# Optimization experiments

Hardware: AMD Instinct MI355X
Metric: run time of the kernel (lower is better)

Reference implementation:

```python
import jax, jax.numpy as jnp
import numpy as np

B, S, HID, NH = 4, 2048, 1024, 16
DH = HID // NH  # 64
SCALE = 1.0 / float(np.sqrt(DH))


def _linear_params(key, scale=0.02):
    kw, kb = jax.random.split(key)
    W = jax.random.normal(kw, (HID, HID), dtype=jnp.float32) * scale
    b = jax.random.normal(kb, (HID,), dtype=jnp.float32) * scale
    return W, b


def setup_inputs() -> dict:
    key = jax.random.key(0)
    ks = jax.random.split(key, 9)
    x = jax.random.normal(ks[0], (B, S, HID), dtype=jnp.float32)
    reasoning_mask = jax.random.uniform(ks[1], (B, S, 1, 1), dtype=jnp.float32)
    Wq, bq = _linear_params(ks[2])
    Wk, bk = _linear_params(ks[3])
    Wv, bv = _linear_params(ks[4])
    Wqr, bqr = _linear_params(ks[5])
    Wkr, bkr = _linear_params(ks[6])
    Wo, bo = _linear_params(ks[7])
    return {"x": x, "reasoning_mask": reasoning_mask,
            "Wq": Wq, "bq": bq, "Wk": Wk, "bk": bk, "Wv": Wv, "bv": bv,
            "Wqr": Wqr, "bqr": bqr, "Wkr": Wkr, "bkr": bkr, "Wo": Wo, "bo": bo}


def reference(x, reasoning_mask, Wq, bq, Wk, bk, Wv, bv, Wqr, bqr, Wkr, bkr, Wo, bo):
    # Projections: x @ W + b, then view (B, S, NH, DH)
    def proj(W, b):
        return (jnp.einsum('bsh,hd->bsd', x, W) + b).reshape(B, S, NH, DH)

    q = proj(Wq, bq)
    k = proj(Wk, bk)
    v = proj(Wv, bv)
    q_r = proj(Wqr, bqr)
    k_r = proj(Wkr, bkr)

    # Reasoning-gated blend of standard and reasoning projections
    q = q * (1.0 - reasoning_mask) + q_r * reasoning_mask
    k = k * (1.0 - reasoning_mask) + k_r * reasoning_mask

    # Faithful to source: matmul over the LAST two dims of (B,S,NH,DH),
    # i.e. per-token attention ACROSS HEADS -> scores shape (B,S,NH,NH)
    scores = jnp.einsum('bshd,bsed->bshe', q, k) * SCALE
    attn = jax.nn.softmax(scores, axis=-1)  # dropout is identity at eval
    out = jnp.einsum('bshe,bsed->bshd', attn, v)  # (B,S,NH,DH)

    # Faithful transpose(1,2) + contiguous view to (B, S, HID)
    out = jnp.transpose(out, (0, 2, 1, 3)).reshape(B, -1, HID)
    return jnp.einsum('bsh,hd->bsd', out, Wo) + bo
```

## Files before the change

kernel.cpp:

```cpp
#include <hip/hip_runtime.h>
#include <hip/hip_bf16.h>


typedef __attribute__((ext_vector_type(8))) short short8;
typedef __attribute__((ext_vector_type(4))) short short4v;
typedef __attribute__((ext_vector_type(4))) float f32x4;

#define HID 1024
#define NTOK 8192
#define WT_ELEMS (1024 * 1024)

__device__ __forceinline__ short f2bs(float f) {
  __hip_bfloat16 h = __float2bfloat16(f);
  return *reinterpret_cast<short*>(&h);
}
__device__ __forceinline__ float bs2f(short s) {
  __hip_bfloat16 h;
  *reinterpret_cast<short*>(&h) = s;
  return __bfloat162float(h);
}
__device__ __forceinline__ void gload16(const void* g, void* l) {
  __builtin_amdgcn_global_load_lds(
      (const __attribute__((address_space(1))) void*)g,
      (__attribute__((address_space(3))) void*)l, 16, 0, 0);
}

#define BAR() asm volatile("s_barrier" ::: "memory")
#define VMWAIT(N) asm volatile("s_waitcnt vmcnt(" #N ")" ::: "memory")
#define LGKMW(N) do { asm volatile("s_waitcnt lgkmcnt(" #N ")" ::: "memory"); \
                      __builtin_amdgcn_sched_barrier(0); } while (0)
#define SCB __builtin_amdgcn_sched_barrier(0)
#define PRIO1 __builtin_amdgcn_s_setprio(1)
#define PRIO0 __builtin_amdgcn_s_setprio(0)
#define MFMA16x16 __builtin_amdgcn_mfma_f32_16x16x32_bf16

__global__ __launch_bounds__(256) void prep_kernel(
    const float* __restrict__ W0, const float* __restrict__ W1,
    const float* __restrict__ W2, const float* __restrict__ W3,
    const float* __restrict__ W4, const float* __restrict__ W5,
    const float* __restrict__ X, short* __restrict__ WT, short* __restrict__ XB)
{
  __shared__ short sT[64][68];
  const int bid = blockIdx.x, tid = threadIdx.x;
  if (bid < 1536) {
    const int z = bid >> 8, rem = bid & 255;
    const float* W = z == 0 ? W0 : z == 1 ? W1 : z == 2 ? W2 : z == 3 ? W3
                   : z == 4 ? W4 : W5;
    short* OUT = WT + (size_t)z * WT_ELEMS;
    const int k0 = (rem & 15) * 64, n0 = (rem >> 4) * 64;
    #pragma unroll
    for (int i = 0; i < 4; i++) {
      const int li = tid + i * 256;
      const int kr = li >> 4, c4 = (li & 15) << 2;
      const f32x4 wv = *reinterpret_cast<const f32x4*>(&W[(size_t)(k0 + kr) * HID + n0 + c4]);
      short4v s4;
      #pragma unroll
      for (int j = 0; j < 4; j++) s4[j] = f2bs(wv[j]);
      *reinterpret_cast<short4v*>(&sT[kr][c4]) = s4;
    }
    __syncthreads();
    #pragma unroll
    for (int i = 0; i < 4; i++) {
      const int li = tid + i * 256;
      const int nr = li >> 4, k4 = (li & 15) << 2;
      short4v o;
      #pragma unroll
      for (int j = 0; j < 4; j++) o[j] = sT[k4 + j][nr];
      const int kcol = (k0 + k4) ^ ((nr & 7) << 3);
      *reinterpret_cast<short4v*>(&OUT[(size_t)(n0 + nr) * HID + kcol]) = o;
    }
  } else {
    const int gid = (bid - 1536) * 256 + tid;
    const int row = gid >> 7, kc = (gid & 127) << 3;
    const f32x4 a = *reinterpret_cast<const f32x4*>(&X[(size_t)row * HID + kc]);
    const f32x4 b = *reinterpret_cast<const f32x4*>(&X[(size_t)row * HID + kc + 4]);
    short8 s;
    #pragma unroll
    for (int j = 0; j < 4; j++) { s[j] = f2bs(a[j]); s[4 + j] = f2bs(b[j]); }
    const int phys = (kc & ~63) | ((kc & 63) ^ ((row & 7) << 3));
    *reinterpret_cast<short8*>(&XB[(size_t)row * HID + phys]) = s;
  }
}

__global__ __launch_bounds__(512, 2) void gated8_kernel(
    const short* __restrict__ XB, const short* __restrict__ WTbase,
    const float* __restrict__ bq, const float* __restrict__ bqr,
    const float* __restrict__ bk, const float* __restrict__ bkr,
    const float* __restrict__ MASK,
    __hip_bfloat16* __restrict__ qg, __hip_bfloat16* __restrict__ kg)
{
  __shared__ short lA[2][256][64];
  __shared__ short lB1[2][128][64];
  __shared__ short lB2[2][128][64];

  const int d = blockIdx.x;
  const int bx = d & 31, byz = d >> 5;
  const int by = byz & 7, z = byz >> 3;

  const short* W1T = WTbase + (size_t)(2 * z) * WT_ELEMS;
  const short* W2T = W1T + WT_ELEMS;
  const float* B1b = z ? bk : bq;
  const float* B2b = z ? bkr : bqr;
  __hip_bfloat16* OUT = z ? kg : qg;

  const int m0 = bx * 256, n0 = by * 128;
  const int tid = threadIdx.x, lane = tid & 63, w = tid >> 6;
  const int wr = (w >> 1) * 64, wc = (w & 1) * 64;
  const int lrow = lane & 15, lkhi = (lane >> 4) << 3;
  const int swz = (lrow & 7) << 3;
  const int srow = lane >> 3, scol = (lane & 7) << 3;

  f32x4 acc1[4][4] = {}, acc2[4][4] = {};
  short8 bf1k[4], bf2k[4], bf1b[4];
  short8 afA0, afA1, afA2, afA3;
  short8 afB0, afB1, afB2, afB3;

  auto stA2 = [&](int slot, int kt, int i0) {
    const int k0 = kt * 64;
    #pragma unroll
    for (int i = 0; i < 2; i++) {
      const int chunk = w * 4 + i0 + i;
      gload16(&XB[(size_t)(m0 + chunk * 8 + srow) * HID + k0 + scol],
              &lA[slot][chunk * 8][0]);
    }
  };
  auto stB1s = [&](int slot, int kt) {
    const int k0 = kt * 64;
    #pragma unroll
    for (int i = 0; i < 2; i++) {
      const int chunk = w * 2 + i;
      gload16(&W1T[(size_t)(n0 + chunk * 8 + srow) * HID + k0 + scol],
              &lB1[slot][chunk * 8][0]);
    }
  };
  auto stB2s = [&](int slot, int kt) {
    const int k0 = kt * 64;
    #pragma unroll
    for (int i = 0; i < 2; i++) {
      const int chunk = w * 2 + i;
      gload16(&W2T[(size_t)(n0 + chunk * 8 + srow) * HID + k0 + scol],
              &lB2[slot][chunk * 8][0]);
    }
  };
  auto rdA = [&](int s, int m, int kk) -> short8 {
    const int lk = (kk * 32 + lkhi) ^ swz;
    return *reinterpret_cast<const short8*>(&lA[s][wr + m * 16 + lrow][lk]);
  };

#define RDB1(DST, S, KK)                                                              \
  _Pragma("unroll")                                                                   \
  for (int n = 0; n < 4; n++) {                                                       \
    const int lk = ((KK) * 32 + lkhi) ^ swz;                                          \
    DST[n] = *reinterpret_cast<const short8*>(&lB1[S][wc + n * 16 + lrow][lk]);       \
  }
#define RDB2(DST, S, KK)                                                              \
  _Pragma("unroll")                                                                   \
  for (int n = 0; n < 4; n++) {                                                       \
    const int lk = ((KK) * 32 + lkhi) ^ swz;                                          \
    DST[n] = *reinterpret_cast<const short8*>(&lB2[S][wc + n * 16 + lrow][lk]);       \
  }
#define MMC1(A0, A1, A2, A3, BF)                                          \
  _Pragma("unroll")                                                       \
  for (int n = 0; n < 4; n++) {                                           \
    acc1[0][n] = MFMA16x16(A0, BF[n], acc1[0][n], 0, 0, 0);               \
    acc1[1][n] = MFMA16x16(A1, BF[n], acc1[1][n], 0, 0, 0);               \
    acc1[2][n] = MFMA16x16(A2, BF[n], acc1[2][n], 0, 0, 0);               \
    acc1[3][n] = MFMA16x16(A3, BF[n], acc1[3][n], 0, 0, 0);               \
  }
#define MMC2(A0, A1, A2, A3, BF)                                          \
  _Pragma("unroll")                                                       \
  for (int n = 0; n < 4; n++) {                                           \
    acc2[0][n] = MFMA16x16(A0, BF[n], acc2[0][n], 0, 0, 0);               \
    acc2[1][n] = MFMA16x16(A1, BF[n], acc2[1][n], 0, 0, 0);               \
    acc2[2][n] = MFMA16x16(A2, BF[n], acc2[2][n], 0, 0, 0);               \
    acc2[3][n] = MFMA16x16(A3, BF[n], acc2[3][n], 0, 0, 0);               \
  }
#define GTILE(S, SN, TS)                                                 \
  afA0 = rdA(S, 0, 0); afA1 = rdA(S, 1, 0);                              \
  afA2 = rdA(S, 2, 0); afA3 = rdA(S, 3, 0);                              \
  SCB;                                                                   \
  RDB1(bf1k, S, 0);                                                      \
  SCB;                                                                   \
  RDB2(bf2k, S, 0);                                                      \
  SCB;                                                                   \
  afB0 = rdA(S, 0, 1); afB1 = rdA(S, 1, 1);                              \
  afB2 = rdA(S, 2, 1); afB3 = rdA(S, 3, 1);                              \
  SCB;                                                                   \
  RDB1(bf1b, S, 1);                                                      \
  SCB;                                                                   \
  stA2(SN, TS, 0); stA2(SN, TS, 2); stB1s(SN, TS); stB2s(SN, TS);        \
  SCB;                                                                   \
  LGKMW(12);                                                             \
  PRIO1; MMC1(afA0, afA1, afA2, afA3, bf1k) PRIO0; SCB;                  \
  LGKMW(8);                                                              \
  PRIO1; MMC2(afA0, afA1, afA2, afA3, bf2k) PRIO0; SCB;                  \
  RDB2(bf2k, S, 1);                                                      \
  SCB;                                                                   \
  LGKMW(4);                                                              \
  PRIO1; MMC1(afB0, afB1, afB2, afB3, bf1b) PRIO0; SCB;                  \
  LGKMW(0);                                                              \
  PRIO1; MMC2(afB0, afB1, afB2, afB3, bf2k) PRIO0; SCB;                  \
  VMWAIT(0);                                                             \
  BAR();

  stA2(0, 0, 0); stA2(0, 0, 2); stB1s(0, 0); stB2s(0, 0);
  VMWAIT(0);
  BAR();

  #pragma unroll 1
  for (int i = 0; i < 16; i++) {
    const int S = i & 1, SN = S ^ 1;
    const int TS = (i < 15) ? i + 1 : 15;
    GTILE(S, SN, TS)
  }
#undef GTILE
#undef MMC1
#undef MMC2
#undef RDB1
#undef RDB2

  #pragma unroll
  for (int m = 0; m < 4; m++) {
    const int rbase = m0 + wr + m * 16 + ((lane >> 4) << 2);
    #pragma unroll
    for (int n = 0; n < 4; n++) {
      const int col = n0 + wc + n * 16 + lrow;
      const float bias1 = B1b[col];
      const float bias2 = B2b[col];
      #pragma unroll
      for (int r = 0; r < 4; r++) {
        const int row = rbase + r;
        const float mk = MASK[row];
        const float val = (acc1[m][n][r] + bias1) * (1.f - mk) +
                          (acc2[m][n][r] + bias2) * mk;
        OUT[(size_t)row * HID + col] = __float2bfloat16(val);
      }
    }
  }
}

template<bool OUTF32>
__global__ __launch_bounds__(512, 2) void plain8_kernel(
    const short* __restrict__ A, const short* __restrict__ WT,
    const float* __restrict__ BIAS, void* __restrict__ OUTv)
{
  __shared__ short lA[3][256][64];
  __shared__ short lB[3][128][64];

  const int d = blockIdx.x;
  const int bx = d & 31, by = d >> 5;

  const int m0 = bx * 256, n0 = by * 128;
  const int tid = threadIdx.x, lane = tid & 63, w = tid >> 6;
  const int wr = (w >> 1) * 64, wc = (w & 1) * 64;
  const int lrow = lane & 15, lkhi = (lane >> 4) << 3;
  const int swz = (lrow & 7) << 3;
  const int srow = lane >> 3, scol = (lane & 7) << 3;

  f32x4 acc[4][4] = {};
  short8 paf[2][4], pbf[2][4];

  auto stTrip = [&](int slot, int kt, int t) {
    const int k0 = kt * 64;
    if (t == 0) {
      #pragma unroll
      for (int i = 0; i < 3; i++) {
        const int chunk = w * 4 + i;
        gload16(&A[(size_t)(m0 + chunk * 8 + srow) * HID + k0 + scol],
                &lA[slot][chunk * 8][0]);
      }
    } else {
      const int chunk = w * 4 + 3;
      gload16(&A[(size_t)(m0 + chunk * 8 + srow) * HID + k0 + scol],
              &lA[slot][chunk * 8][0]);
      #pragma unroll
      for (int i = 0; i < 2; i++) {
        const int bchunk = w * 2 + i;
        gload16(&WT[(size_t)(n0 + bchunk * 8 + srow) * HID + k0 + scol],
                &lB[slot][bchunk * 8][0]);
      }
    }
  };

#define RDP(S, KK)                                                                    \
  _Pragma("unroll")                                                                   \
  for (int m = 0; m < 4; m++) {                                                       \
    const int lk = ((KK) * 32 + lkhi) ^ swz;                                          \
    paf[KK][m] = *reinterpret_cast<const short8*>(&lA[S][wr + m * 16 + lrow][lk]);    \
    pbf[KK][m] = *reinterpret_cast<const short8*>(&lB[S][wc + m * 16 + lrow][lk]);    \
  }
#define PMM16(KK)                                                                     \
  _Pragma("unroll")                                                                   \
  for (int m = 0; m < 4; m++)                                                         \
    _Pragma("unroll")                                                                 \
    for (int n = 0; n < 4; n++)                                                       \
      acc[m][n] = MFMA16x16(paf[KK][m], pbf[KK][n], acc[KK == 0 ? m : m][n], 0, 0, 0);

  stTrip(0, 0, 0); stTrip(0, 0, 1);
  stTrip(1, 1, 0); stTrip(1, 1, 1);
  VMWAIT(6);
  BAR();

  int s = 0, s2 = 2;
  #pragma unroll 1
  for (int t = 0; t < 16; t++) {
    const int TS = (t < 14) ? t + 2 : 15;
    RDP(s, 0)
    SCB;
    RDP(s, 1)
    SCB;
    stTrip(s2, TS, 0); stTrip(s2, TS, 1);
    SCB;
    LGKMW(8);
    PRIO1; PMM16(0) PRIO0; SCB;
    LGKMW(0);
    PRIO1; PMM16(1) PRIO0; SCB;
    VMWAIT(6);
    BAR();
    s = (s == 2) ? 0 : s + 1;
    s2 = (s2 == 2) ? 0 : s2 + 1;
  }
#undef PMM16
#undef RDP

  #pragma unroll
  for (int m = 0; m < 4; m++) {
    const int rbase = m0 + wr + m * 16 + ((lane >> 4) << 2);
    #pragma unroll
    for (int n = 0; n < 4; n++) {
      const int col = n0 + wc + n * 16 + lrow;
      const float bias = BIAS[col];
      #pragma unroll
      for (int r = 0; r < 4; r++) {
        const float val = acc[m][n][r] + bias;
        const size_t oidx = (size_t)(rbase + r) * HID + col;
        if (OUTF32) ((float*)OUTv)[oidx] = val;
        else ((__hip_bfloat16*)OUTv)[oidx] = __float2bfloat16(val);
      }
    }
  }
}

__global__ __launch_bounds__(256) void attn_kernel(
    const __hip_bfloat16* __restrict__ Q, const __hip_bfloat16* __restrict__ K,
    const __hip_bfloat16* __restrict__ V, __hip_bfloat16* __restrict__ O)
{
  const int t = blockIdx.x;
  const int b = t >> 11, s = t & 2047;
  __shared__ float sQ[16][68], sK[16][68], sV[16][68];
  __shared__ float sA[16][17];
  const int tid = threadIdx.x;
  const size_t tb = (size_t)t * HID;

  {
    const int h = tid >> 4, d0 = (tid & 15) << 2;
    const int o = (h << 6) + d0;
    const short4v qv = *reinterpret_cast<const short4v*>(&((const short*)Q)[tb + o]);
    const short4v kv = *reinterpret_cast<const short4v*>(&((const short*)K)[tb + o]);
    const short4v vv = *reinterpret_cast<const short4v*>(&((const short*)V)[tb + o]);
    #pragma unroll
    for (int j = 0; j < 4; j++) {
      sQ[h][d0 + j] = bs2f(qv[j]);
      sK[h][d0 + j] = bs2f(kv[j]);
      sV[h][d0 + j] = bs2f(vv[j]);
    }
  }
  __syncthreads();

  const int h = tid >> 4, e = tid & 15;
  float sc = 0.f;
  #pragma unroll
  for (int dd = 0; dd < 64; dd++) sc += sQ[h][dd] * sK[e][dd];
  sc *= 0.125f;

  float mx = sc;
  mx = fmaxf(mx, __shfl_xor(mx, 1));
  mx = fmaxf(mx, __shfl_xor(mx, 2));
  mx = fmaxf(mx, __shfl_xor(mx, 4));
  mx = fmaxf(mx, __shfl_xor(mx, 8));
  const float p = __expf(sc - mx);
  float sm = p;
  sm += __shfl_xor(sm, 1);
  sm += __shfl_xor(sm, 2);
  sm += __shfl_xor(sm, 4);
  sm += __shfl_xor(sm, 8);
  sA[h][e] = p / sm;
  __syncthreads();

  const int row7 = (s >> 4) & 7;
  const size_t ob = ((size_t)b * 2048 + (s >> 4)) * HID + ((size_t)(s & 15) << 6);
  {
    const int hh = tid >> 4, d4 = (tid & 15) << 2;
    f32x4 o = {0.f, 0.f, 0.f, 0.f};
    #pragma unroll
    for (int e2 = 0; e2 < 16; e2++) {
      const float a = sA[hh][e2];
      #pragma unroll
      for (int j = 0; j < 4; j++) o[j] += a * sV[e2][d4 + j];
    }
    short4v ov;
    #pragma unroll
    for (int j = 0; j < 4; j++) ov[j] = f2bs(o[j]);
    *reinterpret_cast<short4v*>(
        &((short*)O)[ob + (size_t)hh * 128 * HID + (d4 ^ (row7 << 3))]) = ov;
  }
}

extern "C" void kernel_launch(void* const* d_in, const int* in_sizes, int n_in,
                              void* d_out, int out_size, void* d_ws, size_t ws_size,
                              hipStream_t stream) {
  (void)in_sizes; (void)n_in; (void)out_size; (void)ws_size;
  const float* x   = (const float*)d_in[0];
  const float* rm  = (const float*)d_in[1];
  const float* Wq  = (const float*)d_in[2];
  const float* bq  = (const float*)d_in[3];
  const float* Wk  = (const float*)d_in[4];
  const float* bk  = (const float*)d_in[5];
  const float* Wv  = (const float*)d_in[6];
  const float* bv  = (const float*)d_in[7];
  const float* Wqr = (const float*)d_in[8];
  const float* bqr = (const float*)d_in[9];
  const float* Wkr = (const float*)d_in[10];
  const float* bkr = (const float*)d_in[11];
  const float* Wo  = (const float*)d_in[12];
  const float* bo  = (const float*)d_in[13];

  char* ws = (char*)d_ws;
  short* wt = (short*)ws;
  __hip_bfloat16* qg = (__hip_bfloat16*)(ws + 12u * 1024 * 1024);
  __hip_bfloat16* vv = (__hip_bfloat16*)(ws + 28u * 1024 * 1024);
  __hip_bfloat16* ar = (__hip_bfloat16*)(ws + 44u * 1024 * 1024);
  short* xb = (short*)d_out;
  __hip_bfloat16* kg = (__hip_bfloat16*)((char*)d_out + 16u * 1024 * 1024);

  prep_kernel<<<dim3(5632), 256, 0, stream>>>(Wq, Wqr, Wk, Wkr, Wv, Wo, x, wt, xb);
  gated8_kernel<<<dim3(512), 512, 0, stream>>>(xb, wt, bq, bqr, bk, bkr, rm, qg, kg);
  plain8_kernel<false><<<dim3(256), 512, 0, stream>>>(xb, wt + (size_t)4 * WT_ELEMS, bv, vv);
  attn_kernel<<<dim3(NTOK), 256, 0, stream>>>(qg, kg, vv, ar);
  plain8_kernel<true><<<dim3(256), 512, 0, stream>>>((const short*)ar,
                                                     wt + (size_t)5 * WT_ELEMS, bo, d_out);
}
```

Measured before the change: 145.2 us.

## Merge V projection into gated Q/K projection launch and move barriers before last MFMA

```diff
diff --git a/kernel.cpp b/kernel.cpp
--- a/kernel.cpp
+++ b/kernel.cpp
@@ -82,26 +82,26 @@
   }
 }
 
-__global__ __launch_bounds__(512, 2) void gated8_kernel(
+__global__ __launch_bounds__(512, 2) void proj_kernel(
     const short* __restrict__ XB, const short* __restrict__ WTbase,
     const float* __restrict__ bq, const float* __restrict__ bqr,
     const float* __restrict__ bk, const float* __restrict__ bkr,
-    const float* __restrict__ MASK,
-    __hip_bfloat16* __restrict__ qg, __hip_bfloat16* __restrict__ kg)
+    const float* __restrict__ bv, const float* __restrict__ MASK,
+    __hip_bfloat16* __restrict__ qg, __hip_bfloat16* __restrict__ kg,
+    __hip_bfloat16* __restrict__ vg)
 {
   __shared__ short lA[2][256][64];
   __shared__ short lB1[2][128][64];
   __shared__ short lB2[2][128][64];
 
-  const int d = blockIdx.x;
-  const int bx = d & 31, byz = d >> 5;
-  const int by = byz & 7, z = byz >> 3;
-
-  const short* W1T = WTbase + (size_t)(2 * z) * WT_ELEMS;
+  const int z = blockIdx.z;
+  const int bx = blockIdx.x & 31, by = blockIdx.x >> 5;
+  const bool gated = (z < 2);
+  const short* W1T = WTbase + (size_t)(z == 2 ? 4 : 2 * z) * WT_ELEMS;
   const short* W2T = W1T + WT_ELEMS;
-  const float* B1b = z ? bk : bq;
-  const float* B2b = z ? bkr : bqr;
-  __hip_bfloat16* OUT = z ? kg : qg;
+  const float* B1b = z == 0 ? bq : z == 1 ? bk : bv;
+  const float* B2b = z == 0 ? bqr : bkr;
+  __hip_bfloat16* OUT = z == 0 ? qg : z == 1 ? kg : vg;
 
   const int m0 = bx * 256, n0 = by * 128;
   const int tid = threadIdx.x, lane = tid & 63, w = tid >> 6;
@@ -111,7 +111,7 @@
   const int srow = lane >> 3, scol = (lane & 7) << 3;
 
   f32x4 acc1[4][4] = {}, acc2[4][4] = {};
-  short8 bf1k[4], bf2k[4], bf1b[4];
+  short8 bfa[4], bfb[4];
   short8 afA0, afA1, afA2, afA3;
   short8 afB0, afB1, afB2, afB3;
 
@@ -147,17 +147,11 @@
     return *reinterpret_cast<const short8*>(&lA[s][wr + m * 16 + lrow][lk]);
   };
 
-#define RDB1(DST, S, KK)                                                              \
+#define RDBF(DST, LB, S, KK)                                                          \
   _Pragma("unroll")                                                                   \
   for (int n = 0; n < 4; n++) {                                                       \
     const int lk = ((KK) * 32 + lkhi) ^ swz;                                          \
-    DST[n] = *reinterpret_cast<const short8*>(&lB1[S][wc + n * 16 + lrow][lk]);       \
-  }
-#define RDB2(DST, S, KK)                                                              \
-  _Pragma("unroll")                                                                   \
-  for (int n = 0; n < 4; n++) {                                                       \
-    const int lk = ((KK) * 32 + lkhi) ^ swz;                                          \
-    DST[n] = *reinterpret_cast<const short8*>(&lB2[S][wc + n * 16 + lrow][lk]);       \
+    DST[n] = *reinterpret_cast<const short8*>(&LB[S][wc + n * 16 + lrow][lk]);        \
   }
 #define MMC1(A0, A1, A2, A3, BF)                                          \
   _Pragma("unroll")                                                       \
@@ -177,47 +171,66 @@
   }
 #define GTILE(S, SN, TS)                                                 \
   afA0 = rdA(S, 0, 0); afA1 = rdA(S, 1, 0);                              \
-  afA2 = rdA(S, 2, 0); afA3 = rdA(S, 3, 0);                              \
-  SCB;                                                                   \
-  RDB1(bf1k, S, 0);                                                      \
-  SCB;                                                                   \
-  RDB2(bf2k, S, 0);                                                      \
-  SCB;                                                                   \
+  afA2 = rdA(S, 2, 0); afA3 = rdA(S, 3, 0); SCB;                         \
+  RDBF(bfa, lB1, S, 0); SCB;                                             \
+  RDBF(bfb, lB2, S, 0); SCB;                                             \
   afB0 = rdA(S, 0, 1); afB1 = rdA(S, 1, 1);                              \
-  afB2 = rdA(S, 2, 1); afB3 = rdA(S, 3, 1);                              \
-  SCB;                                                                   \
-  RDB1(bf1b, S, 1);                                                      \
-  SCB;                                                                   \
-  stA2(SN, TS, 0); stA2(SN, TS, 2); stB1s(SN, TS); stB2s(SN, TS);        \
-  SCB;                                                                   \
-  LGKMW(12);                                                             \
-  PRIO1; MMC1(afA0, afA1, afA2, afA3, bf1k) PRIO0; SCB;                  \
+  afB2 = rdA(S, 2, 1); afB3 = rdA(S, 3, 1); SCB;                         \
+  stA2(SN, TS, 0); stA2(SN, TS, 2); stB1s(SN, TS); stB2s(SN, TS); SCB;   \
   LGKMW(8);                                                              \
-  PRIO1; MMC2(afA0, afA1, afA2, afA3, bf2k) PRIO0; SCB;                  \
-  RDB2(bf2k, S, 1);                                                      \
-  SCB;                                                                   \
+  PRIO1; MMC1(afA0, afA1, afA2, afA3, bfa) PRIO0; SCB;                   \
+  RDBF(bfa, lB1, S, 1); SCB;                                             \
+  LGKMW(8);                                                              \
+  PRIO1; MMC2(afA0, afA1, afA2, afA3, bfb) PRIO0; SCB;                   \
+  RDBF(bfb, lB2, S, 1); SCB;                                             \
   LGKMW(4);                                                              \
-  PRIO1; MMC1(afB0, afB1, afB2, afB3, bf1b) PRIO0; SCB;                  \
+  PRIO1; MMC1(afB0, afB1, afB2, afB3, bfa) PRIO0; SCB;                   \
   LGKMW(0);                                                              \
-  PRIO1; MMC2(afB0, afB1, afB2, afB3, bf2k) PRIO0; SCB;                  \
   VMWAIT(0);                                                             \
-  BAR();
-
-  stA2(0, 0, 0); stA2(0, 0, 2); stB1s(0, 0); stB2s(0, 0);
+  BAR();                                                                 \
+  PRIO1; MMC2(afB0, afB1, afB2, afB3, bfb) PRIO0; SCB;
+#define PTILE(S, SN, TS)                                                 \
+  afA0 = rdA(S, 0, 0); afA1 = rdA(S, 1, 0);                              \
+  afA2 = rdA(S, 2, 0); afA3 = rdA(S, 3, 0); SCB;                         \
+  RDBF(bfa, lB1, S, 0); SCB;                                             \
+  afB0 = rdA(S, 0, 1); afB1 = rdA(S, 1, 1);                              \
+  afB2 = rdA(S, 2, 1); afB3 = rdA(S, 3, 1); SCB;                         \
+  RDBF(bfb, lB1, S, 1); SCB;                                             \
+  stA2(SN, TS, 0); stA2(SN, TS, 2); stB1s(SN, TS); SCB;                  \
+  LGKMW(8);                                                              \
+  PRIO1; MMC1(afA0, afA1, afA2, afA3, bfa) PRIO0; SCB;                   \
+  LGKMW(0);                                                              \
+  VMWAIT(0);                                                             \
+  BAR();                                                                 \
+  PRIO1; MMC1(afB0, afB1, afB2, afB3, bfb) PRIO0; SCB;
+
+  if (gated) {
+    stA2(0, 0, 0); stA2(0, 0, 2); stB1s(0, 0); stB2s(0, 0);
+    VMWAIT(0);
+    BAR();
+    #pragma unroll 1
+    for (int i = 0; i < 16; i++) {
+      const int S = i & 1, SN = S ^ 1;
+      const int TS = (i < 15) ? i + 1 : 15;
+      GTILE(S, SN, TS)
+    }
+  } else {
+    stA2(0, 0, 0); stA2(0, 0, 2); stB1s(0, 0);
+    VMWAIT(0);
+    BAR();
+    #pragma unroll 1
+    for (int i = 0; i < 16; i++) {
+      const int S = i & 1, SN = S ^ 1;
+      const int TS = (i < 15) ? i + 1 : 15;
+      PTILE(S, SN, TS)
+    }
+  }
   VMWAIT(0);
-  BAR();
-
-  #pragma unroll 1
-  for (int i = 0; i < 16; i++) {
-    const int S = i & 1, SN = S ^ 1;
-    const int TS = (i < 15) ? i + 1 : 15;
-    GTILE(S, SN, TS)
-  }
 #undef GTILE
+#undef PTILE
 #undef MMC1
 #undef MMC2
-#undef RDB1
-#undef RDB2
+#undef RDBF
 
   #pragma unroll
   for (int m = 0; m < 4; m++) {
@@ -226,23 +239,24 @@
     for (int n = 0; n < 4; n++) {
       const int col = n0 + wc + n * 16 + lrow;
       const float bias1 = B1b[col];
-      const float bias2 = B2b[col];
+      const float bias2 = gated ? B2b[col] : 0.f;
       #pragma unroll
       for (int r = 0; r < 4; r++) {
         const int row = rbase + r;
-        const float mk = MASK[row];
-        const float val = (acc1[m][n][r] + bias1) * (1.f - mk) +
-                          (acc2[m][n][r] + bias2) * mk;
+        float val = acc1[m][n][r] + bias1;
+        if (gated) {
+          const float mk = MASK[row];
+          val = val * (1.f - mk) + (acc2[m][n][r] + bias2) * mk;
+        }
         OUT[(size_t)row * HID + col] = __float2bfloat16(val);
       }
     }
   }
 }
 
-template<bool OUTF32>
-__global__ __launch_bounds__(512, 2) void plain8_kernel(
+__global__ __launch_bounds__(512, 2) void out_kernel(
     const short* __restrict__ A, const short* __restrict__ WT,
-    const float* __restrict__ BIAS, void* __restrict__ OUTv)
+    const float* __restrict__ BIAS, float* __restrict__ OUT)
 {
   __shared__ short lA[3][256][64];
   __shared__ short lB[3][128][64];
@@ -294,7 +308,7 @@
   for (int m = 0; m < 4; m++)                                                         \
     _Pragma("unroll")                                                                 \
     for (int n = 0; n < 4; n++)                                                       \
-      acc[m][n] = MFMA16x16(paf[KK][m], pbf[KK][n], acc[KK == 0 ? m : m][n], 0, 0, 0);
+      acc[m][n] = MFMA16x16(paf[KK][m], pbf[KK][n], acc[m][n], 0, 0, 0);
 
   stTrip(0, 0, 0); stTrip(0, 0, 1);
   stTrip(1, 1, 0); stTrip(1, 1, 1);
@@ -314,12 +328,13 @@
     LGKMW(8);
     PRIO1; PMM16(0) PRIO0; SCB;
     LGKMW(0);
-    PRIO1; PMM16(1) PRIO0; SCB;
     VMWAIT(6);
     BAR();
+    PRIO1; PMM16(1) PRIO0; SCB;
     s = (s == 2) ? 0 : s + 1;
     s2 = (s2 == 2) ? 0 : s2 + 1;
   }
+  VMWAIT(0);
 #undef PMM16
 #undef RDP
 
@@ -331,12 +346,8 @@
       const int col = n0 + wc + n * 16 + lrow;
       const float bias = BIAS[col];
       #pragma unroll
-      for (int r = 0; r < 4; r++) {
-        const float val = acc[m][n][r] + bias;
-        const size_t oidx = (size_t)(rbase + r) * HID + col;
-        if (OUTF32) ((float*)OUTv)[oidx] = val;
-        else ((__hip_bfloat16*)OUTv)[oidx] = __float2bfloat16(val);
-      }
+      for (int r = 0; r < 4; r++)
+        OUT[(size_t)(rbase + r) * HID + col] = acc[m][n][r] + bias;
     }
   }
 }
@@ -434,9 +445,9 @@
   __hip_bfloat16* kg = (__hip_bfloat16*)((char*)d_out + 16u * 1024 * 1024);
 
   prep_kernel<<<dim3(5632), 256, 0, stream>>>(Wq, Wqr, Wk, Wkr, Wv, Wo, x, wt, xb);
-  gated8_kernel<<<dim3(512), 512, 0, stream>>>(xb, wt, bq, bqr, bk, bkr, rm, qg, kg);
-  plain8_kernel<false><<<dim3(256), 512, 0, stream>>>(xb, wt + (size_t)4 * WT_ELEMS, bv, vv);
+  proj_kernel<<<dim3(256, 1, 3), 512, 0, stream>>>(xb, wt, bq, bqr, bk, bkr, bv, rm,
+                                                   qg, kg, vv);
   attn_kernel<<<dim3(NTOK), 256, 0, stream>>>(qg, kg, vv, ar);
-  plain8_kernel<true><<<dim3(256), 512, 0, stream>>>((const short*)ar,
-                                                     wt + (size_t)5 * WT_ELEMS, bo, d_out);
-}
+  out_kernel<<<dim3(256), 512, 0, stream>>>((const short*)ar, wt + (size_t)5 * WT_ELEMS,
+                                            bo, (float*)d_out);
+}
```

Measured after the change: 156.5 us. +7.8%, slower.

## Reschedule dual-GEMM tile loop into barrier-separated phases with staggered loads

Applied to the files above, without the earlier changes.

```diff
diff --git a/kernel.cpp b/kernel.cpp
--- a/kernel.cpp
+++ b/kernel.cpp
@@ -27,9 +27,6 @@
 
 #define BAR() asm volatile("s_barrier" ::: "memory")
 #define VMWAIT(N) asm volatile("s_waitcnt vmcnt(" #N ")" ::: "memory")
-#define LGKMW(N) do { asm volatile("s_waitcnt lgkmcnt(" #N ")" ::: "memory"); \
-                      __builtin_amdgcn_sched_barrier(0); } while (0)
-#define SCB __builtin_amdgcn_sched_barrier(0)
 #define PRIO1 __builtin_amdgcn_s_setprio(1)
 #define PRIO0 __builtin_amdgcn_s_setprio(0)
 #define MFMA16x16 __builtin_amdgcn_mfma_f32_16x16x32_bf16
@@ -111,7 +108,7 @@
   const int srow = lane >> 3, scol = (lane & 7) << 3;
 
   f32x4 acc1[4][4] = {}, acc2[4][4] = {};
-  short8 bf1k[4], bf2k[4], bf1b[4];
+  short8 bfa[4], bfb[4];
   short8 afA0, afA1, afA2, afA3;
   short8 afB0, afB1, afB2, afB3;
 
@@ -176,35 +173,37 @@
     acc2[3][n] = MFMA16x16(A3, BF[n], acc2[3][n], 0, 0, 0);               \
   }
 #define GTILE(S, SN, TS)                                                 \
+                                                                 \
   afA0 = rdA(S, 0, 0); afA1 = rdA(S, 1, 0);                              \
   afA2 = rdA(S, 2, 0); afA3 = rdA(S, 3, 0);                              \
-  SCB;                                                                   \
-  RDB1(bf1k, S, 0);                                                      \
-  SCB;                                                                   \
-  RDB2(bf2k, S, 0);                                                      \
-  SCB;                                                                   \
+  RDB1(bfa, S, 0);                                                       \
+  stA2(SN, TS, 0); stA2(SN, TS, 2);                                      \
+  VMWAIT(4);                                                             \
+  BAR();                                                                 \
+  PRIO1; MMC1(afA0, afA1, afA2, afA3, bfa) PRIO0;                        \
+  BAR();                                                                 \
+                                                                 \
+  RDB2(bfb, S, 0);                                                       \
+  stB1s(SN, TS); stB2s(SN, TS);                                          \
+  BAR();                                                                 \
+  PRIO1; MMC2(afA0, afA1, afA2, afA3, bfb) PRIO0;                        \
+  BAR();                                                                 \
+                                                                 \
   afB0 = rdA(S, 0, 1); afB1 = rdA(S, 1, 1);                              \
   afB2 = rdA(S, 2, 1); afB3 = rdA(S, 3, 1);                              \
-  SCB;                                                                   \
-  RDB1(bf1b, S, 1);                                                      \
-  SCB;                                                                   \
-  stA2(SN, TS, 0); stA2(SN, TS, 2); stB1s(SN, TS); stB2s(SN, TS);        \
-  SCB;                                                                   \
-  LGKMW(12);                                                             \
-  PRIO1; MMC1(afA0, afA1, afA2, afA3, bf1k) PRIO0; SCB;                  \
-  LGKMW(8);                                                              \
-  PRIO1; MMC2(afA0, afA1, afA2, afA3, bf2k) PRIO0; SCB;                  \
-  RDB2(bf2k, S, 1);                                                      \
-  SCB;                                                                   \
-  LGKMW(4);                                                              \
-  PRIO1; MMC1(afB0, afB1, afB2, afB3, bf1b) PRIO0; SCB;                  \
-  LGKMW(0);                                                              \
-  PRIO1; MMC2(afB0, afB1, afB2, afB3, bf2k) PRIO0; SCB;                  \
-  VMWAIT(0);                                                             \
+  RDB1(bfa, S, 1);                                                       \
+  BAR();                                                                 \
+  PRIO1; MMC1(afB0, afB1, afB2, afB3, bfa) PRIO0;                        \
+  BAR();                                                                 \
+                                                                 \
+  RDB2(bfb, S, 1);                                                       \
+  VMWAIT(2);                                                             \
+  BAR();                                                                 \
+  PRIO1; MMC2(afB0, afB1, afB2, afB3, bfb) PRIO0;                        \
   BAR();
 
   stA2(0, 0, 0); stA2(0, 0, 2); stB1s(0, 0); stB2s(0, 0);
-  VMWAIT(0);
+  VMWAIT(2);
   BAR();
 
   #pragma unroll 1
@@ -213,6 +212,7 @@
     const int TS = (i < 15) ? i + 1 : 15;
     GTILE(S, SN, TS)
   }
+  VMWAIT(0);
 #undef GTILE
 #undef MMC1
 #undef MMC2
@@ -294,7 +294,7 @@
   for (int m = 0; m < 4; m++)                                                         \
     _Pragma("unroll")                                                                 \
     for (int n = 0; n < 4; n++)                                                       \
-      acc[m][n] = MFMA16x16(paf[KK][m], pbf[KK][n], acc[KK == 0 ? m : m][n], 0, 0, 0);
+      acc[m][n] = MFMA16x16(paf[KK][m], pbf[KK][n], acc[m][n], 0, 0, 0);
 
   stTrip(0, 0, 0); stTrip(0, 0, 1);
   stTrip(1, 1, 0); stTrip(1, 1, 1);
@@ -306,20 +306,15 @@
   for (int t = 0; t < 16; t++) {
     const int TS = (t < 14) ? t + 2 : 15;
     RDP(s, 0)
-    SCB;
     RDP(s, 1)
-    SCB;
     stTrip(s2, TS, 0); stTrip(s2, TS, 1);
-    SCB;
-    LGKMW(8);
-    PRIO1; PMM16(0) PRIO0; SCB;
-    LGKMW(0);
-    PRIO1; PMM16(1) PRIO0; SCB;
+    PRIO1; PMM16(0) PMM16(1) PRIO0;
     VMWAIT(6);
     BAR();
     s = (s == 2) ? 0 : s + 1;
     s2 = (s2 == 2) ? 0 : s2 + 1;
   }
+  VMWAIT(0);
 #undef PMM16
 #undef RDP
 
```

New measurement: 149.7 us. 1.03x slower.
